# Performance work log

Hardware: AMD Instinct MI355X
Metric: run time of the kernel (lower is better)

The kernel has to match this reference:

```python
import jax, jax.numpy as jnp
import numpy as np

IN_F, T_IN, T_OUT = 8, 96, 32
B = 4096


def _lstm(x, Wih, Whh, b):
    """Standard LSTM (torch gate order i,f,g,o), batch_first. x: [B,T,I] -> [B,T,H].
    Variational dropout with p=0 (eval mode) is identity, so omitted."""
    Bsz = x.shape[0]
    H = Whh.shape[1]
    # precompute input contribution for all timesteps: [B,T,4H]
    xg = jnp.einsum('bti,gi->btg', x, Wih) + b

    def step(carry, xt):
        h, c = carry
        g = xt + h @ Whh.T  # [B,4H]
        i, f, gg, o = jnp.split(g, 4, axis=-1)
        c = jax.nn.sigmoid(f) * c + jax.nn.sigmoid(i) * jnp.tanh(gg)
        h = jax.nn.sigmoid(o) * jnp.tanh(c)
        return (h, c), h

    h0 = jnp.zeros((Bsz, H), x.dtype)
    _, ys = jax.lax.scan(step, (h0, h0), jnp.swapaxes(xg, 0, 1))
    return jnp.swapaxes(ys, 0, 1)


def setup_inputs() -> dict:
    key = jax.random.key(0)
    ks = jax.random.split(key, 16)
    s = 0.1  # init scale
    return {
        'x': jax.random.normal(ks[0], (B, T_IN, IN_F), jnp.float32),
        'e1_Wih': s * jax.random.normal(ks[1], (256, IN_F), jnp.float32),
        'e1_Whh': s * jax.random.normal(ks[2], (256, 64), jnp.float32),
        'e1_b': s * jax.random.normal(ks[3], (256,), jnp.float32),
        'e2_Wih': s * jax.random.normal(ks[4], (4, 64), jnp.float32),
        'e2_Whh': s * jax.random.normal(ks[5], (4, 1), jnp.float32),
        'e2_b': s * jax.random.normal(ks[6], (4,), jnp.float32),
        'd1_Wih': s * jax.random.normal(ks[7], (64, 1), jnp.float32),
        'd1_Whh': s * jax.random.normal(ks[8], (64, 16), jnp.float32),
        'd1_b': s * jax.random.normal(ks[9], (64,), jnp.float32),
        'd2_Wih': s * jax.random.normal(ks[10], (4, 16), jnp.float32),
        'd2_Whh': s * jax.random.normal(ks[11], (4, 1), jnp.float32),
        'd2_b': s * jax.random.normal(ks[12], (4,), jnp.float32),
        'fc1_W': s * jax.random.normal(ks[13], (32, T_IN + T_OUT), jnp.float32),
        'fc1_b': s * jax.random.normal(ks[13], (32,), jnp.float32),
        'fc2_W': s * jax.random.normal(ks[14], (T_OUT, 32), jnp.float32),
        'fc2_b': s * jax.random.normal(ks[15], (T_OUT,), jnp.float32),
    }


def reference(x, e1_Wih, e1_Whh, e1_b, e2_Wih, e2_Whh, e2_b,
              d1_Wih, d1_Whh, d1_b, d2_Wih, d2_Whh, d2_b,
              fc1_W, fc1_b, fc2_W, fc2_b):
    # Encoder: LSTM(in->64) -> LSTM(64->1) -> ReLU
    h = _lstm(x, e1_Wih, e1_Whh, e1_b)
    h = _lstm(h, e2_Wih, e2_Whh, e2_b)
    enc_out = jax.nn.relu(h)  # [B, T_IN, 1]
    # Auxiliary: last T_OUT steps of invocation column (col 0)
    x_aux = x[:, -T_OUT:, 0:1]  # [B, T_OUT, 1]
    dec_in = jnp.concatenate([enc_out, x_aux], axis=1)  # [B, T_IN+T_OUT, 1]
    # Decoder: LSTM(1->16) -> LSTM(16->1)
    d = _lstm(dec_in, d1_Wih, d1_Whh, d1_b)
    d = _lstm(d, d2_Wih, d2_Whh, d2_b)  # [B, T_IN+T_OUT, 1]
    # FC head over the flattened time dim
    flat = d.reshape(-1, T_IN + T_OUT)
    out = flat @ fc1_W.T + fc1_b
    out = out @ fc2_W.T + fc2_b
    return out  # [B, T_OUT]
```

## Files before the change

### kernel.cpp

```cpp
#include <hip/hip_runtime.h>
#include <hip/hip_bf16.h>

typedef __attribute__((ext_vector_type(8))) short bf16x8;
typedef __attribute__((ext_vector_type(4))) float f32x4;

__device__ __forceinline__ float sigm(float x) {
    return __builtin_amdgcn_rcpf(1.0f + __expf(-x));
}
__device__ __forceinline__ float tanh_(float x) {
    float e = __expf(2.0f * x);
    return 1.0f - 2.0f * __builtin_amdgcn_rcpf(e + 1.0f);
}
__device__ __forceinline__ ushort f2bf(float f) {
    uint u = __float_as_uint(f);
    u = u + 0x7FFFu + ((u >> 16) & 1u);
    return (ushort)(u >> 16);
}
__device__ __forceinline__ float bf2f(ushort s) { return __uint_as_float(((uint)s) << 16); }

__global__ __launch_bounds__(1024) __attribute__((amdgpu_waves_per_eu(4, 4)))
void fused_all(
    const float* __restrict__ x,
    const float* __restrict__ e1_Wih, const float* __restrict__ e1_Whh, const float* __restrict__ e1_b,
    const float* __restrict__ e2_Wih, const float* __restrict__ e2_b,
    const float* __restrict__ e2_Whh,
    const float* __restrict__ d1_Wih, const float* __restrict__ d1_Whh, const float* __restrict__ d1_b,
    const float* __restrict__ d2_Wih, const float* __restrict__ d2_b,
    const float* __restrict__ d2_Whh,
    const float* __restrict__ fc1_W, const float* __restrict__ fc1_b,
    const float* __restrict__ fc2_W, const float* __restrict__ fc2_b,
    float* __restrict__ out)
{
    __shared__ float x_s[16 * 772];
    __shared__ __align__(16) ushort h_hi[2][8][16][8];
    __shared__ __align__(16) ushort h_lo[2][8][16][8];
    __shared__ __align__(16) ushort x2_s[2][4][16][8];
    __shared__ __align__(16) float pe2_s[96 * 64];
    __shared__ float din_s[16][132];
    __shared__ float h_lds[16][16];
    __shared__ float pd2_s[16 * 516];
    __shared__ float d2h_s[16 * 132];
    __shared__ float mid_s[16 * 36];

    const int t = threadIdx.x;
    const int bBase = blockIdx.x * 16;
    const int wv = t >> 6, l = t & 63;
    const int row = l & 15, sub = l >> 4;

    for (int bb = 0; bb < 16; ++bb)
        for (int i = t; i < 768; i += 1024)
            x_s[bb * 772 + i] = x[(size_t)(bBase + bb) * 768 + i];

    auto loadW = [&](const float* rowbase, int k0, bool valid, bf16x8& hi8, bf16x8& lo8) {
        float f[8];
        if (valid) {
            float4 v0 = ((const float4*)(rowbase + k0))[0];
            float4 v1 = ((const float4*)(rowbase + k0))[1];
            f[0]=v0.x; f[1]=v0.y; f[2]=v0.z; f[3]=v0.w;
            f[4]=v1.x; f[5]=v1.y; f[6]=v1.z; f[7]=v1.w;
        } else {
            #pragma unroll
            for (int j = 0; j < 8; ++j) f[j] = 0.f;
        }
        #pragma unroll
        for (int j = 0; j < 8; ++j) {
            ushort h = f2bf(f[j]);
            hi8[j] = (short)h;
            lo8[j] = (short)f2bf(f[j] - bf2f(h));
        }
    };
    auto loadA = [&](int T, bool isE2, bf16x8& Ah0, bf16x8& Ah1, bf16x8& Al0, bf16x8& Al1, bf16x8& A2) {
        const int gate = row & 3, uq = row >> 2;
        const bool valid = !isE2 || (uq == 0);
        const int wr = isE2 ? gate : gate * 64 + T * 4 + uq;
        const float* rp = isE2 ? (e2_Wih + (size_t)wr * 64) : (e1_Whh + (size_t)wr * 64);
        loadW(rp, sub * 8,      valid, Ah0, Al0);
        loadW(rp, 32 + sub * 8, valid, Ah1, Al1);
        #pragma unroll
        for (int j = 0; j < 8; ++j) A2[j] = 0;
        if (valid) {
            if (!isE2) {
                if (sub < 3) {
                    const float* wihr = e1_Wih + (size_t)wr * 8;
                    #pragma unroll
                    for (int j = 0; j < 8; ++j) {
                        float f = wihr[j];
                        ushort hh = f2bf(f);
                        A2[j] = (sub < 2) ? (short)hh : (short)f2bf(f - bf2f(hh));
                    }
                } else {
                    float bb = e1_b[wr];
                    ushort hh = f2bf(bb);
                    A2[0] = (short)hh; A2[1] = (short)f2bf(bb - bf2f(hh));
                }
            } else if (sub == 3) {
                float bb = e2_b[wr];
                ushort hh = f2bf(bb);
                A2[0] = (short)hh; A2[1] = (short)f2bf(bb - bf2f(hh));
            }
        }
    };

    bf16x8 A0h0, A0h1, A0l0, A0l1, A0x;
    bf16x8 A2h0, A2h1, A2l0, A2l1, A2x;
    loadA(wv, false, A0h0, A0h1, A0l0, A0l1, A0x);
    if (wv == 15) loadA(0, true, A2h0, A2h1, A2l0, A2l1, A2x);

    __syncthreads();

    if (t < 1024) { ((ushort*)h_hi[0])[t] = 0; ((ushort*)h_lo[0])[t] = 0; }
    if (t < 384) {
        int sb = t >> 7, b = (t >> 3) & 15, j = t & 7;
        float xv = x_s[b * 772 + j];
        ushort hi = f2bf(xv);
        x2_s[0][sb][b][j] = (sb == 1) ? f2bf(xv - bf2f(hi)) : hi;
        x2_s[1][sb][b][j] = 0;
    } else if (t < 512) {
        int b = (t >> 3) & 15, j = t & 7;
        ushort v = (j < 2) ? (ushort)0x3F80 : (ushort)0;
        x2_s[0][3][b][j] = v;
        x2_s[1][3][b][j] = v;
    }

    const int cb = l & 15;
    const int u0_ = wv * 4 + sub;
    float c0r = 0.f;
    __syncthreads();

    #pragma unroll 1
    for (int ts = 0; ts < 96; ++ts) {
        const int p = ts & 1, pn = p ^ 1;

        bf16x8 Bh0 = *(const bf16x8*)&h_hi[p][sub][cb][0];
        bf16x8 Bh1 = *(const bf16x8*)&h_hi[p][4 + sub][cb][0];
        bf16x8 Bl0 = *(const bf16x8*)&h_lo[p][sub][cb][0];
        bf16x8 Bl1 = *(const bf16x8*)&h_lo[p][4 + sub][cb][0];
        bf16x8 Bx  = *(const bf16x8*)&x2_s[p][sub][cb][0];

        f32x4 u0 = {0.f,0.f,0.f,0.f}, v0 = {0.f,0.f,0.f,0.f};
        u0 = __builtin_amdgcn_mfma_f32_16x16x32_bf16(A0h0, Bh0, u0, 0, 0, 0);
        u0 = __builtin_amdgcn_mfma_f32_16x16x32_bf16(A0l0, Bh0, u0, 0, 0, 0);
        u0 = __builtin_amdgcn_mfma_f32_16x16x32_bf16(A0h0, Bl0, u0, 0, 0, 0);
        v0 = __builtin_amdgcn_mfma_f32_16x16x32_bf16(A0h1, Bh1, v0, 0, 0, 0);
        v0 = __builtin_amdgcn_mfma_f32_16x16x32_bf16(A0l1, Bh1, v0, 0, 0, 0);
        v0 = __builtin_amdgcn_mfma_f32_16x16x32_bf16(A0h1, Bl1, v0, 0, 0, 0);
        v0 = __builtin_amdgcn_mfma_f32_16x16x32_bf16(A0x,  Bx,  v0, 0, 0, 0);

        if (wv == 15) {
            f32x4 u2 = {0.f,0.f,0.f,0.f}, v2 = {0.f,0.f,0.f,0.f};
            u2 = __builtin_amdgcn_mfma_f32_16x16x32_bf16(A2h0, Bh0, u2, 0, 0, 0);
            u2 = __builtin_amdgcn_mfma_f32_16x16x32_bf16(A2l0, Bh0, u2, 0, 0, 0);
            u2 = __builtin_amdgcn_mfma_f32_16x16x32_bf16(A2h0, Bl0, u2, 0, 0, 0);
            v2 = __builtin_amdgcn_mfma_f32_16x16x32_bf16(A2h1, Bh1, v2, 0, 0, 0);
            v2 = __builtin_amdgcn_mfma_f32_16x16x32_bf16(A2l1, Bh1, v2, 0, 0, 0);
            v2 = __builtin_amdgcn_mfma_f32_16x16x32_bf16(A2h1, Bl1, v2, 0, 0, 0);
            v2 = __builtin_amdgcn_mfma_f32_16x16x32_bf16(A2x,  Bx,  v2, 0, 0, 0);
            if (ts > 0 && sub == 0) {
                f32x4 acc2 = u2 + v2;
                #pragma unroll
                for (int i = 0; i < 4; ++i)
                    pe2_s[(ts - 1) * 64 + i * 16 + cb] = acc2[i];
            }
        }

        {
            f32x4 acc = u0 + v0;
            c0r = fmaf(sigm(acc[1]), c0r, sigm(acc[0]) * tanh_(acc[2]));
            float hv = sigm(acc[3]) * tanh_(c0r);
            ushort hh = f2bf(hv);
            h_hi[pn][u0_ >> 3][cb][u0_ & 7] = hh;
            h_lo[pn][u0_ >> 3][cb][u0_ & 7] = f2bf(hv - bf2f(hh));
        }

        if (ts < 95 && t < 384) {
            int sb = t >> 7, b = (t >> 3) & 15, j = t & 7;
            float xv = x_s[b * 772 + (ts + 1) * 8 + j];
            ushort hi = f2bf(xv);
            x2_s[pn][sb][b][j] = (sb == 1) ? f2bf(xv - bf2f(hi)) : hi;
        }
        __syncthreads();
    }

    if (wv == 15) {
        bf16x8 Bh0 = *(const bf16x8*)&h_hi[0][sub][cb][0];
        bf16x8 Bh1 = *(const bf16x8*)&h_hi[0][4 + sub][cb][0];
        bf16x8 Bl0 = *(const bf16x8*)&h_lo[0][sub][cb][0];
        bf16x8 Bl1 = *(const bf16x8*)&h_lo[0][4 + sub][cb][0];
        bf16x8 Bx  = *(const bf16x8*)&x2_s[0][sub][cb][0];
        f32x4 u2 = {0.f,0.f,0.f,0.f}, v2 = {0.f,0.f,0.f,0.f};
        u2 = __builtin_amdgcn_mfma_f32_16x16x32_bf16(A2h0, Bh0, u2, 0, 0, 0);
        u2 = __builtin_amdgcn_mfma_f32_16x16x32_bf16(A2l0, Bh0, u2, 0, 0, 0);
        u2 = __builtin_amdgcn_mfma_f32_16x16x32_bf16(A2h0, Bl0, u2, 0, 0, 0);
        v2 = __builtin_amdgcn_mfma_f32_16x16x32_bf16(A2h1, Bh1, v2, 0, 0, 0);
        v2 = __builtin_amdgcn_mfma_f32_16x16x32_bf16(A2l1, Bh1, v2, 0, 0, 0);
        v2 = __builtin_amdgcn_mfma_f32_16x16x32_bf16(A2h1, Bl1, v2, 0, 0, 0);
        v2 = __builtin_amdgcn_mfma_f32_16x16x32_bf16(A2x,  Bx,  v2, 0, 0, 0);
        if (sub == 0) {
            f32x4 acc2 = u2 + v2;
            #pragma unroll
            for (int i = 0; i < 4; ++i)
                pe2_s[95 * 64 + i * 16 + cb] = acc2[i];
        }
    }
    __syncthreads();

    if (wv == 0 && l < 16) {
        const float w0 = e2_Whh[0], w1 = e2_Whh[1], w2 = e2_Whh[2], w3 = e2_Whh[3];
        float ni = pe2_s[l], nf = pe2_s[16 + l], ng = pe2_s[32 + l], no = pe2_s[48 + l];
        float h = 0.f, c = 0.f;
        #pragma unroll 1
        for (int ts = 0; ts < 96; ++ts) {
            float gi = ni, gf = nf, gg2 = ng, go = no;
            if (ts < 95) {
                int b2 = (ts + 1) * 64;
                ni = pe2_s[b2 + l]; nf = pe2_s[b2 + 16 + l];
                ng = pe2_s[b2 + 32 + l]; no = pe2_s[b2 + 48 + l];
            }
            gi = fmaf(h, w0, gi);
            gf = fmaf(h, w1, gf);
            gg2 = fmaf(h, w2, gg2);
            go = fmaf(h, w3, go);
            c = fmaf(sigm(gf), c, sigm(gi) * tanh_(gg2));
            h = sigm(go) * tanh_(c);
            din_s[l][ts] = fmaxf(h, 0.f);
        }
    }
    if (wv >= 1 && wv <= 8) {
        int i = (wv - 1) * 64 + l;
        int B = i >> 5, j = i & 31;
        din_s[B][96 + j] = x_s[B * 772 + (64 + j) * 8];
    }
    __syncthreads();

    {
        const int dw = t >> 6, dlane = t & 63;
        const int dq = dlane >> 4, du = dlane & 15;
        const int drow = dw * 4 + dq;

        if (t < 256) {
            float wih_g[4], bg[4], whh_g[4][16], d2w[16];
            #pragma unroll
            for (int g = 0; g < 4; ++g) {
                wih_g[g] = d1_Wih[g * 16 + du];
                bg[g]    = d1_b[g * 16 + du];
                const float4* wp = (const float4*)(d1_Whh + (size_t)(g * 16 + du) * 16);
                #pragma unroll
                for (int k4 = 0; k4 < 4; ++k4) {
                    float4 v = wp[k4];
                    whh_g[g][4*k4+0] = v.x; whh_g[g][4*k4+1] = v.y;
                    whh_g[g][4*k4+2] = v.z; whh_g[g][4*k4+3] = v.w;
                }
            }
            {
                const float4* wp = (const float4*)(d2_Wih + (size_t)(du & 3) * 16);
                #pragma unroll
                for (int k4 = 0; k4 < 4; ++k4) {
                    float4 v = wp[k4];
                    d2w[4*k4+0] = v.x; d2w[4*k4+1] = v.y; d2w[4*k4+2] = v.z; d2w[4*k4+3] = v.w;
                }
            }
            const float d2bias = d2_b[du & 3];

            float h = 0.f, c = 0.f;
            float hv[16];
            #pragma unroll 1
            for (int ts = 0; ts < 128; ++ts) {
                float xv = din_s[drow][ts];
                float p0 = fmaf(xv, wih_g[0], bg[0]);
                float p1 = fmaf(xv, wih_g[1], bg[1]);
                float p2 = fmaf(xv, wih_g[2], bg[2]);
                float p3 = fmaf(xv, wih_g[3], bg[3]);
                if (ts > 0) {
                    const float4* hp = (const float4*)&h_lds[drow][0];
                    #pragma unroll
                    for (int k4 = 0; k4 < 4; ++k4) {
                        float4 v = hp[k4];
                        hv[4*k4+0] = v.x; hv[4*k4+1] = v.y; hv[4*k4+2] = v.z; hv[4*k4+3] = v.w;
                    }
                    #pragma unroll
                    for (int k = 0; k < 16; ++k) {
                        p0 = fmaf(hv[k], whh_g[0][k], p0);
                        p1 = fmaf(hv[k], whh_g[1][k], p1);
                        p2 = fmaf(hv[k], whh_g[2][k], p2);
                        p3 = fmaf(hv[k], whh_g[3][k], p3);
                    }
                    if (du < 4) {
                        float a = d2bias;
                        #pragma unroll
                        for (int k = 0; k < 16; ++k) a = fmaf(hv[k], d2w[k], a);
                        pd2_s[drow * 516 + (ts - 1) * 4 + du] = a;
                    }
                }
                c = fmaf(sigm(p1), c, sigm(p0) * tanh_(p2));
                h = sigm(p3) * tanh_(c);
                h_lds[drow][du] = h;
            }
            {
                const float4* hp = (const float4*)&h_lds[drow][0];
                #pragma unroll
                for (int k4 = 0; k4 < 4; ++k4) {
                    float4 v = hp[k4];
                    hv[4*k4+0] = v.x; hv[4*k4+1] = v.y; hv[4*k4+2] = v.z; hv[4*k4+3] = v.w;
                }
                if (du < 4) {
                    float a = d2bias;
                    #pragma unroll
                    for (int k = 0; k < 16; ++k) a = fmaf(hv[k], d2w[k], a);
                    pd2_s[drow * 516 + 127 * 4 + du] = a;
                }
            }
        }
        __syncthreads();

        if (t < 16) {
            const float w0 = d2_Whh[0], w1 = d2_Whh[1], w2 = d2_Whh[2], w3 = d2_Whh[3];
            float4 dbuf[4];
            #pragma unroll
            for (int j = 0; j < 4; ++j) dbuf[j] = *(const float4*)&pd2_s[t * 516 + j * 4];
            float h2 = 0.f, c2 = 0.f;
            #pragma unroll
            for (int ts = 0; ts < 128; ++ts) {
                float4 g4 = dbuf[ts & 3];
                if (ts + 4 < 128) dbuf[ts & 3] = *(const float4*)&pd2_s[t * 516 + (ts + 4) * 4];
                float gi = fmaf(h2, w0, g4.x);
                float gf = fmaf(h2, w1, g4.y);
                float gg = fmaf(h2, w2, g4.z);
                float go = fmaf(h2, w3, g4.w);
                c2 = fmaf(sigm(gf), c2, sigm(gi) * tanh_(gg));
                h2 = sigm(go) * tanh_(c2);
                d2h_s[t * 132 + ts] = h2;
            }
        }
        __syncthreads();

        if (t < 256) {
            const int bb = t >> 4, o = t & 15;
            float acc0 = fc1_b[o], acc1 = fc1_b[o + 16];
            const float4* wa = (const float4*)(fc1_W + (size_t)o * 128);
            const float4* wb = (const float4*)(fc1_W + (size_t)(o + 16) * 128);
            const float4* fp = (const float4*)&d2h_s[bb * 132];
            #pragma unroll
            for (int k4 = 0; k4 < 32; ++k4) {
                float4 f = fp[k4], va = wa[k4], vb = wb[k4];
                acc0 = fmaf(f.x, va.x, acc0); acc0 = fmaf(f.y, va.y, acc0);
                acc0 = fmaf(f.z, va.z, acc0); acc0 = fmaf(f.w, va.w, acc0);
                acc1 = fmaf(f.x, vb.x, acc1); acc1 = fmaf(f.y, vb.y, acc1);
                acc1 = fmaf(f.z, vb.z, acc1); acc1 = fmaf(f.w, vb.w, acc1);
            }
            mid_s[bb * 36 + o] = acc0;
            mid_s[bb * 36 + o + 16] = acc1;
        }
        __syncthreads();

        if (t < 256) {
            const int bb = t >> 4, o = t & 15;
            float o0 = fc2_b[o], o1 = fc2_b[o + 16];
            const float4* va2 = (const float4*)(fc2_W + (size_t)o * 32);
            const float4* vb2 = (const float4*)(fc2_W + (size_t)(o + 16) * 32);
            const float4* mp = (const float4*)&mid_s[bb * 36];
            #pragma unroll
            for (int k4 = 0; k4 < 8; ++k4) {
                float4 m = mp[k4], va = va2[k4], vb = vb2[k4];
                o0 = fmaf(m.x, va.x, o0); o0 = fmaf(m.y, va.y, o0);
                o0 = fmaf(m.z, va.z, o0); o0 = fmaf(m.w, va.w, o0);
                o1 = fmaf(m.x, vb.x, o1); o1 = fmaf(m.y, vb.y, o1);
                o1 = fmaf(m.z, vb.z, o1); o1 = fmaf(m.w, vb.w, o1);
            }
            out[((size_t)bBase + bb) * 32 + o] = o0;
            out[((size_t)bBase + bb) * 32 + o + 16] = o1;
        }
    }
}

extern "C" void kernel_launch(void* const* d_in, const int* in_sizes, int n_in,
                              void* d_out, int out_size, void* d_ws, size_t ws_size,
                              hipStream_t stream) {
    const float* x      = (const float*)d_in[0];
    const float* e1_Wih = (const float*)d_in[1];
    const float* e1_Whh = (const float*)d_in[2];
    const float* e1_b   = (const float*)d_in[3];
    const float* e2_Wih = (const float*)d_in[4];
    const float* e2_Whh = (const float*)d_in[5];
    const float* e2_b   = (const float*)d_in[6];
    const float* d1_Wih = (const float*)d_in[7];
    const float* d1_Whh = (const float*)d_in[8];
    const float* d1_b   = (const float*)d_in[9];
    const float* d2_Wih = (const float*)d_in[10];
    const float* d2_Whh = (const float*)d_in[11];
    const float* d2_b   = (const float*)d_in[12];
    const float* fc1_W  = (const float*)d_in[13];
    const float* fc1_b  = (const float*)d_in[14];
    const float* fc2_W  = (const float*)d_in[15];
    const float* fc2_b  = (const float*)d_in[16];
    float* out = (float*)d_out;

    hipLaunchKernelGGL(fused_all, dim3(256), dim3(1024), 0, stream,
                       x, e1_Wih, e1_Whh, e1_b, e2_Wih, e2_b, e2_Whh,
                       d1_Wih, d1_Whh, d1_b, d2_Wih, d2_b, d2_Whh,
                       fc1_W, fc1_b, fc2_W, fc2_b, out);
}
```

Before: 149.7 us.

## Wavefront-pipeline all four LSTM layers in one time loop

```diff
diff --git a/kernel.cpp b/kernel.cpp
--- a/kernel.cpp
+++ b/kernel.cpp
@@ -41,6 +41,7 @@
     __shared__ float pd2_s[16 * 516];
     __shared__ float d2h_s[16 * 132];
     __shared__ float mid_s[16 * 36];
+    __shared__ float w_d1[64][20];
 
     const int t = threadIdx.x;
     const int bBase = blockIdx.x * 16;
@@ -50,6 +51,11 @@
     for (int bb = 0; bb < 16; ++bb)
         for (int i = t; i < 768; i += 1024)
             x_s[bb * 772 + i] = x[(size_t)(bBase + bb) * 768 + i];
+
+    for (int i = t; i < 64 * 18; i += 1024) {
+        int r = i / 18, j = i - r * 18;
+        w_d1[r][j] = (j < 16) ? d1_Whh[r * 16 + j] : ((j == 16) ? d1_Wih[r] : d1_b[r]);
+    }
 
     auto loadW = [&](const float* rowbase, int k0, bool valid, bf16x8& hi8, bf16x8& lo8) {
         float f[8];
@@ -121,254 +127,219 @@
         x2_s[0][3][b][j] = v;
         x2_s[1][3][b][j] = v;
     }
-
-    const int cb = l & 15;
-    const int u0_ = wv * 4 + sub;
-    float c0r = 0.f;
-    __syncthreads();
-
-    #pragma unroll 1
-    for (int ts = 0; ts < 96; ++ts) {
-        const int p = ts & 1, pn = p ^ 1;
-
-        bf16x8 Bh0 = *(const bf16x8*)&h_hi[p][sub][cb][0];
-        bf16x8 Bh1 = *(const bf16x8*)&h_hi[p][4 + sub][cb][0];
-        bf16x8 Bl0 = *(const bf16x8*)&h_lo[p][sub][cb][0];
-        bf16x8 Bl1 = *(const bf16x8*)&h_lo[p][4 + sub][cb][0];
-        bf16x8 Bx  = *(const bf16x8*)&x2_s[p][sub][cb][0];
-
-        f32x4 u0 = {0.f,0.f,0.f,0.f}, v0 = {0.f,0.f,0.f,0.f};
-        u0 = __builtin_amdgcn_mfma_f32_16x16x32_bf16(A0h0, Bh0, u0, 0, 0, 0);
-        u0 = __builtin_amdgcn_mfma_f32_16x16x32_bf16(A0l0, Bh0, u0, 0, 0, 0);
-        u0 = __builtin_amdgcn_mfma_f32_16x16x32_bf16(A0h0, Bl0, u0, 0, 0, 0);
-        v0 = __builtin_amdgcn_mfma_f32_16x16x32_bf16(A0h1, Bh1, v0, 0, 0, 0);
-        v0 = __builtin_amdgcn_mfma_f32_16x16x32_bf16(A0l1, Bh1, v0, 0, 0, 0);
-        v0 = __builtin_amdgcn_mfma_f32_16x16x32_bf16(A0h1, Bl1, v0, 0, 0, 0);
-        v0 = __builtin_amdgcn_mfma_f32_16x16x32_bf16(A0x,  Bx,  v0, 0, 0, 0);
-
-        if (wv == 15) {
-            f32x4 u2 = {0.f,0.f,0.f,0.f}, v2 = {0.f,0.f,0.f,0.f};
-            u2 = __builtin_amdgcn_mfma_f32_16x16x32_bf16(A2h0, Bh0, u2, 0, 0, 0);
-            u2 = __builtin_amdgcn_mfma_f32_16x16x32_bf16(A2l0, Bh0, u2, 0, 0, 0);
-            u2 = __builtin_amdgcn_mfma_f32_16x16x32_bf16(A2h0, Bl0, u2, 0, 0, 0);
-            v2 = __builtin_amdgcn_mfma_f32_16x16x32_bf16(A2h1, Bh1, v2, 0, 0, 0);
-            v2 = __builtin_amdgcn_mfma_f32_16x16x32_bf16(A2l1, Bh1, v2, 0, 0, 0);
-            v2 = __builtin_amdgcn_mfma_f32_16x16x32_bf16(A2h1, Bl1, v2, 0, 0, 0);
-            v2 = __builtin_amdgcn_mfma_f32_16x16x32_bf16(A2x,  Bx,  v2, 0, 0, 0);
-            if (ts > 0 && sub == 0) {
-                f32x4 acc2 = u2 + v2;
-                #pragma unroll
-                for (int i = 0; i < 4; ++i)
-                    pe2_s[(ts - 1) * 64 + i * 16 + cb] = acc2[i];
-            }
-        }
-
-        {
-            f32x4 acc = u0 + v0;
-            c0r = fmaf(sigm(acc[1]), c0r, sigm(acc[0]) * tanh_(acc[2]));
-            float hv = sigm(acc[3]) * tanh_(c0r);
-            ushort hh = f2bf(hv);
-            h_hi[pn][u0_ >> 3][cb][u0_ & 7] = hh;
-            h_lo[pn][u0_ >> 3][cb][u0_ & 7] = f2bf(hv - bf2f(hh));
-        }
-
-        if (ts < 95 && t < 384) {
-            int sb = t >> 7, b = (t >> 3) & 15, j = t & 7;
-            float xv = x_s[b * 772 + (ts + 1) * 8 + j];
-            ushort hi = f2bf(xv);
-            x2_s[pn][sb][b][j] = (sb == 1) ? f2bf(xv - bf2f(hi)) : hi;
-        }
-        __syncthreads();
-    }
-
-    if (wv == 15) {
-        bf16x8 Bh0 = *(const bf16x8*)&h_hi[0][sub][cb][0];
-        bf16x8 Bh1 = *(const bf16x8*)&h_hi[0][4 + sub][cb][0];
-        bf16x8 Bl0 = *(const bf16x8*)&h_lo[0][sub][cb][0];
-        bf16x8 Bl1 = *(const bf16x8*)&h_lo[0][4 + sub][cb][0];
-        bf16x8 Bx  = *(const bf16x8*)&x2_s[0][sub][cb][0];
-        f32x4 u2 = {0.f,0.f,0.f,0.f}, v2 = {0.f,0.f,0.f,0.f};
-        u2 = __builtin_amdgcn_mfma_f32_16x16x32_bf16(A2h0, Bh0, u2, 0, 0, 0);
-        u2 = __builtin_amdgcn_mfma_f32_16x16x32_bf16(A2l0, Bh0, u2, 0, 0, 0);
-        u2 = __builtin_amdgcn_mfma_f32_16x16x32_bf16(A2h0, Bl0, u2, 0, 0, 0);
-        v2 = __builtin_amdgcn_mfma_f32_16x16x32_bf16(A2h1, Bh1, v2, 0, 0, 0);
-        v2 = __builtin_amdgcn_mfma_f32_16x16x32_bf16(A2l1, Bh1, v2, 0, 0, 0);
-        v2 = __builtin_amdgcn_mfma_f32_16x16x32_bf16(A2h1, Bl1, v2, 0, 0, 0);
-        v2 = __builtin_amdgcn_mfma_f32_16x16x32_bf16(A2x,  Bx,  v2, 0, 0, 0);
-        if (sub == 0) {
-            f32x4 acc2 = u2 + v2;
-            #pragma unroll
-            for (int i = 0; i < 4; ++i)
-                pe2_s[95 * 64 + i * 16 + cb] = acc2[i];
-        }
-    }
-    __syncthreads();
-
-    if (wv == 0 && l < 16) {
-        const float w0 = e2_Whh[0], w1 = e2_Whh[1], w2 = e2_Whh[2], w3 = e2_Whh[3];
-        float ni = pe2_s[l], nf = pe2_s[16 + l], ng = pe2_s[32 + l], no = pe2_s[48 + l];
-        float h = 0.f, c = 0.f;
-        #pragma unroll 1
-        for (int ts = 0; ts < 96; ++ts) {
-            float gi = ni, gf = nf, gg2 = ng, go = no;
-            if (ts < 95) {
-                int b2 = (ts + 1) * 64;
-                ni = pe2_s[b2 + l]; nf = pe2_s[b2 + 16 + l];
-                ng = pe2_s[b2 + 32 + l]; no = pe2_s[b2 + 48 + l];
-            }
-            gi = fmaf(h, w0, gi);
-            gf = fmaf(h, w1, gf);
-            gg2 = fmaf(h, w2, gg2);
-            go = fmaf(h, w3, go);
-            c = fmaf(sigm(gf), c, sigm(gi) * tanh_(gg2));
-            h = sigm(go) * tanh_(c);
-            din_s[l][ts] = fmaxf(h, 0.f);
-        }
-    }
     if (wv >= 1 && wv <= 8) {
         int i = (wv - 1) * 64 + l;
         int B = i >> 5, j = i & 31;
         din_s[B][96 + j] = x_s[B * 772 + (64 + j) * 8];
     }
+
+    const int cb = l & 15;
+    const int u0_ = wv * 4 + sub;
+    float c0r = 0.f;
+
+    const float e2w0 = e2_Whh[0], e2w1 = e2_Whh[1], e2w2 = e2_Whh[2], e2w3 = e2_Whh[3];
+    float h_e2 = 0.f, c_e2 = 0.f;
+
+    const float d2r0 = d2_Whh[0], d2r1 = d2_Whh[1], d2r2 = d2_Whh[2], d2r3 = d2_Whh[3];
+    float h_d2 = 0.f, c_d2 = 0.f;
+
+    const int dw = t >> 6, dlane = t & 63;
+    const int dq = dlane >> 4, du = dlane & 15;
+    const int drow = dw * 4 + dq;
+    float d2w[16];
+    float d2bias = 0.f;
+    if (t < 256) {
+        const float4* wp = (const float4*)(d2_Wih + (size_t)(du & 3) * 16);
+        #pragma unroll
+        for (int k4 = 0; k4 < 4; ++k4) {
+            float4 v = wp[k4];
+            d2w[4*k4+0] = v.x; d2w[4*k4+1] = v.y; d2w[4*k4+2] = v.z; d2w[4*k4+3] = v.w;
+        }
+        d2bias = d2_b[du & 3];
+    }
+    float c_d1 = 0.f;
+
     __syncthreads();
 
-    {
-        const int dw = t >> 6, dlane = t & 63;
-        const int dq = dlane >> 4, du = dlane & 15;
-        const int drow = dw * 4 + dq;
-
-        if (t < 256) {
-            float wih_g[4], bg[4], whh_g[4][16], d2w[16];
-            #pragma unroll
-            for (int g = 0; g < 4; ++g) {
-                wih_g[g] = d1_Wih[g * 16 + du];
-                bg[g]    = d1_b[g * 16 + du];
-                const float4* wp = (const float4*)(d1_Whh + (size_t)(g * 16 + du) * 16);
+    #pragma unroll 1
+    for (int it = 0; it < 133; ++it) {
+        const int p = it & 1, pn = p ^ 1;
+
+        if (it <= 96) {
+            bf16x8 Bh0 = *(const bf16x8*)&h_hi[p][sub][cb][0];
+            bf16x8 Bh1 = *(const bf16x8*)&h_hi[p][4 + sub][cb][0];
+            bf16x8 Bl0 = *(const bf16x8*)&h_lo[p][sub][cb][0];
+            bf16x8 Bl1 = *(const bf16x8*)&h_lo[p][4 + sub][cb][0];
+            bf16x8 Bx  = *(const bf16x8*)&x2_s[p][sub][cb][0];
+
+            if (it < 96) {
+                f32x4 u0 = {0.f,0.f,0.f,0.f}, v0 = {0.f,0.f,0.f,0.f};
+                u0 = __builtin_amdgcn_mfma_f32_16x16x32_bf16(A0h0, Bh0, u0, 0, 0, 0);
+                u0 = __builtin_amdgcn_mfma_f32_16x16x32_bf16(A0l0, Bh0, u0, 0, 0, 0);
+                u0 = __builtin_amdgcn_mfma_f32_16x16x32_bf16(A0h0, Bl0, u0, 0, 0, 0);
+                v0 = __builtin_amdgcn_mfma_f32_16x16x32_bf16(A0h1, Bh1, v0, 0, 0, 0);
+                v0 = __builtin_amdgcn_mfma_f32_16x16x32_bf16(A0l1, Bh1, v0, 0, 0, 0);
+                v0 = __builtin_amdgcn_mfma_f32_16x16x32_bf16(A0h1, Bl1, v0, 0, 0, 0);
+                v0 = __builtin_amdgcn_mfma_f32_16x16x32_bf16(A0x,  Bx,  v0, 0, 0, 0);
+
+                f32x4 acc = u0 + v0;
+                c0r = fmaf(sigm(acc[1]), c0r, sigm(acc[0]) * tanh_(acc[2]));
+                float hv = sigm(acc[3]) * tanh_(c0r);
+                ushort hh = f2bf(hv);
+                h_hi[pn][u0_ >> 3][cb][u0_ & 7] = hh;
+                h_lo[pn][u0_ >> 3][cb][u0_ & 7] = f2bf(hv - bf2f(hh));
+            }
+            if (wv == 15) {
+                f32x4 u2 = {0.f,0.f,0.f,0.f}, v2 = {0.f,0.f,0.f,0.f};
+                u2 = __builtin_amdgcn_mfma_f32_16x16x32_bf16(A2h0, Bh0, u2, 0, 0, 0);
+                u2 = __builtin_amdgcn_mfma_f32_16x16x32_bf16(A2l0, Bh0, u2, 0, 0, 0);
+                u2 = __builtin_amdgcn_mfma_f32_16x16x32_bf16(A2h0, Bl0, u2, 0, 0, 0);
+                v2 = __builtin_amdgcn_mfma_f32_16x16x32_bf16(A2h1, Bh1, v2, 0, 0, 0);
+                v2 = __builtin_amdgcn_mfma_f32_16x16x32_bf16(A2l1, Bh1, v2, 0, 0, 0);
+                v2 = __builtin_amdgcn_mfma_f32_16x16x32_bf16(A2h1, Bl1, v2, 0, 0, 0);
+                v2 = __builtin_amdgcn_mfma_f32_16x16x32_bf16(A2x,  Bx,  v2, 0, 0, 0);
+                if (it > 0 && sub == 0) {
+                    f32x4 acc2 = u2 + v2;
+                    #pragma unroll
+                    for (int i = 0; i < 4; ++i)
+                        pe2_s[(it - 1) * 64 + i * 16 + cb] = acc2[i];
+                }
+            }
+            if (it < 95 && t < 384) {
+                int sb = t >> 7, b = (t >> 3) & 15, j = t & 7;
+                float xv = x_s[b * 772 + (it + 1) * 8 + j];
+                ushort hi = f2bf(xv);
+                x2_s[pn][sb][b][j] = (sb == 1) ? f2bf(xv - bf2f(hi)) : hi;
+            }
+        }
+
+        if (wv == 4 && l < 16 && it >= 2 && it <= 97) {
+            int s = it - 2;
+            float gi = pe2_s[s * 64 + l];
+            float gf = pe2_s[s * 64 + 16 + l];
+            float gg = pe2_s[s * 64 + 32 + l];
+            float go = pe2_s[s * 64 + 48 + l];
+            gi = fmaf(h_e2, e2w0, gi);
+            gf = fmaf(h_e2, e2w1, gf);
+            gg = fmaf(h_e2, e2w2, gg);
+            go = fmaf(h_e2, e2w3, go);
+            c_e2 = fmaf(sigm(gf), c_e2, sigm(gi) * tanh_(gg));
+            h_e2 = sigm(go) * tanh_(c_e2);
+            din_s[l][s] = fmaxf(h_e2, 0.f);
+        }
+
+        if (t < 256 && it >= 3 && it <= 130) {
+            int s = it - 3;
+            float xv = din_s[drow][s];
+            float wg0[16], wg1[16], wg2[16], wg3[16];
+            {
+                const float4* w0p = (const float4*)&w_d1[du][0];
+                const float4* w1p = (const float4*)&w_d1[16 + du][0];
+                const float4* w2p = (const float4*)&w_d1[32 + du][0];
+                const float4* w3p = (const float4*)&w_d1[48 + du][0];
                 #pragma unroll
                 for (int k4 = 0; k4 < 4; ++k4) {
-                    float4 v = wp[k4];
-                    whh_g[g][4*k4+0] = v.x; whh_g[g][4*k4+1] = v.y;
-                    whh_g[g][4*k4+2] = v.z; whh_g[g][4*k4+3] = v.w;
-                }
-            }
-            {
-                const float4* wp = (const float4*)(d2_Wih + (size_t)(du & 3) * 16);
-                #pragma unroll
-                for (int k4 = 0; k4 < 4; ++k4) {
-                    float4 v = wp[k4];
-                    d2w[4*k4+0] = v.x; d2w[4*k4+1] = v.y; d2w[4*k4+2] = v.z; d2w[4*k4+3] = v.w;
-                }
-            }
-            const float d2bias = d2_b[du & 3];
-
-            float h = 0.f, c = 0.f;
-            float hv[16];
-            #pragma unroll 1
-            for (int ts = 0; ts < 128; ++ts) {
-                float xv = din_s[drow][ts];
-                float p0 = fmaf(xv, wih_g[0], bg[0]);
-                float p1 = fmaf(xv, wih_g[1], bg[1]);
-                float p2 = fmaf(xv, wih_g[2], bg[2]);
-                float p3 = fmaf(xv, wih_g[3], bg[3]);
-                if (ts > 0) {
-                    const float4* hp = (const float4*)&h_lds[drow][0];
-                    #pragma unroll
-                    for (int k4 = 0; k4 < 4; ++k4) {
-                        float4 v = hp[k4];
-                        hv[4*k4+0] = v.x; hv[4*k4+1] = v.y; hv[4*k4+2] = v.z; hv[4*k4+3] = v.w;
-                    }
-                    #pragma unroll
-                    for (int k = 0; k < 16; ++k) {
-                        p0 = fmaf(hv[k], whh_g[0][k], p0);
-                        p1 = fmaf(hv[k], whh_g[1][k], p1);
-                        p2 = fmaf(hv[k], whh_g[2][k], p2);
-                        p3 = fmaf(hv[k], whh_g[3][k], p3);
-                    }
-                    if (du < 4) {
-                        float a = d2bias;
-                        #pragma unroll
-                        for (int k = 0; k < 16; ++k) a = fmaf(hv[k], d2w[k], a);
-                        pd2_s[drow * 516 + (ts - 1) * 4 + du] = a;
-                    }
-                }
-                c = fmaf(sigm(p1), c, sigm(p0) * tanh_(p2));
-                h = sigm(p3) * tanh_(c);
-                h_lds[drow][du] = h;
-            }
-            {
+                    float4 a = w0p[k4]; wg0[4*k4+0]=a.x; wg0[4*k4+1]=a.y; wg0[4*k4+2]=a.z; wg0[4*k4+3]=a.w;
+                    float4 b = w1p[k4]; wg1[4*k4+0]=b.x; wg1[4*k4+1]=b.y; wg1[4*k4+2]=b.z; wg1[4*k4+3]=b.w;
+                    float4 c4 = w2p[k4]; wg2[4*k4+0]=c4.x; wg2[4*k4+1]=c4.y; wg2[4*k4+2]=c4.z; wg2[4*k4+3]=c4.w;
+                    float4 d4 = w3p[k4]; wg3[4*k4+0]=d4.x; wg3[4*k4+1]=d4.y; wg3[4*k4+2]=d4.z; wg3[4*k4+3]=d4.w;
+                }
+            }
+            float p0 = fmaf(xv, w_d1[du][16],      w_d1[du][17]);
+            float p1 = fmaf(xv, w_d1[16 + du][16], w_d1[16 + du][17]);
+            float p2 = fmaf(xv, w_d1[32 + du][16], w_d1[32 + du][17]);
+            float p3 = fmaf(xv, w_d1[48 + du][16], w_d1[48 + du][17]);
+            if (s > 0) {
+                float hv[16];
                 const float4* hp = (const float4*)&h_lds[drow][0];
                 #pragma unroll
                 for (int k4 = 0; k4 < 4; ++k4) {
                     float4 v = hp[k4];
                     hv[4*k4+0] = v.x; hv[4*k4+1] = v.y; hv[4*k4+2] = v.z; hv[4*k4+3] = v.w;
                 }
+                #pragma unroll
+                for (int k = 0; k < 16; ++k) {
+                    p0 = fmaf(hv[k], wg0[k], p0);
+                    p1 = fmaf(hv[k], wg1[k], p1);
+                    p2 = fmaf(hv[k], wg2[k], p2);
+                    p3 = fmaf(hv[k], wg3[k], p3);
+                }
                 if (du < 4) {
                     float a = d2bias;
                     #pragma unroll
                     for (int k = 0; k < 16; ++k) a = fmaf(hv[k], d2w[k], a);
-                    pd2_s[drow * 516 + 127 * 4 + du] = a;
-                }
-            }
-        }
+                    pd2_s[drow * 516 + (s - 1) * 4 + du] = a;
+                }
+            }
+            c_d1 = fmaf(sigm(p1), c_d1, sigm(p0) * tanh_(p2));
+            float h = sigm(p3) * tanh_(c_d1);
+            h_lds[drow][du] = h;
+        }
+        if (t < 256 && it == 131) {
+            float hv[16];
+            const float4* hp = (const float4*)&h_lds[drow][0];
+            #pragma unroll
+            for (int k4 = 0; k4 < 4; ++k4) {
+                float4 v = hp[k4];
+                hv[4*k4+0] = v.x; hv[4*k4+1] = v.y; hv[4*k4+2] = v.z; hv[4*k4+3] = v.w;
+            }
+            if (du < 4) {
+                float a = d2bias;
+                #pragma unroll
+                for (int k = 0; k < 16; ++k) a = fmaf(hv[k], d2w[k], a);
+                pd2_s[drow * 516 + 127 * 4 + du] = a;
+            }
+        }
+
+        if (wv == 5 && l < 16 && it >= 5) {
+            int s = it - 5;
+            float4 g4 = *(const float4*)&pd2_s[l * 516 + s * 4];
+            float gi = fmaf(h_d2, d2r0, g4.x);
+            float gf = fmaf(h_d2, d2r1, g4.y);
+            float gg = fmaf(h_d2, d2r2, g4.z);
+            float go = fmaf(h_d2, d2r3, g4.w);
+            c_d2 = fmaf(sigm(gf), c_d2, sigm(gi) * tanh_(gg));
+            h_d2 = sigm(go) * tanh_(c_d2);
+            d2h_s[l * 132 + s] = h_d2;
+        }
+
         __syncthreads();
-
-        if (t < 16) {
-            const float w0 = d2_Whh[0], w1 = d2_Whh[1], w2 = d2_Whh[2], w3 = d2_Whh[3];
-            float4 dbuf[4];
-            #pragma unroll
-            for (int j = 0; j < 4; ++j) dbuf[j] = *(const float4*)&pd2_s[t * 516 + j * 4];
-            float h2 = 0.f, c2 = 0.f;
-            #pragma unroll
-            for (int ts = 0; ts < 128; ++ts) {
-                float4 g4 = dbuf[ts & 3];
-                if (ts + 4 < 128) dbuf[ts & 3] = *(const float4*)&pd2_s[t * 516 + (ts + 4) * 4];
-                float gi = fmaf(h2, w0, g4.x);
-                float gf = fmaf(h2, w1, g4.y);
-                float gg = fmaf(h2, w2, g4.z);
-                float go = fmaf(h2, w3, g4.w);
-                c2 = fmaf(sigm(gf), c2, sigm(gi) * tanh_(gg));
-                h2 = sigm(go) * tanh_(c2);
-                d2h_s[t * 132 + ts] = h2;
-            }
-        }
-        __syncthreads();
-
-        if (t < 256) {
-            const int bb = t >> 4, o = t & 15;
-            float acc0 = fc1_b[o], acc1 = fc1_b[o + 16];
-            const float4* wa = (const float4*)(fc1_W + (size_t)o * 128);
-            const float4* wb = (const float4*)(fc1_W + (size_t)(o + 16) * 128);
-            const float4* fp = (const float4*)&d2h_s[bb * 132];
-            #pragma unroll
-            for (int k4 = 0; k4 < 32; ++k4) {
-                float4 f = fp[k4], va = wa[k4], vb = wb[k4];
-                acc0 = fmaf(f.x, va.x, acc0); acc0 = fmaf(f.y, va.y, acc0);
-                acc0 = fmaf(f.z, va.z, acc0); acc0 = fmaf(f.w, va.w, acc0);
-                acc1 = fmaf(f.x, vb.x, acc1); acc1 = fmaf(f.y, vb.y, acc1);
-                acc1 = fmaf(f.z, vb.z, acc1); acc1 = fmaf(f.w, vb.w, acc1);
-            }
-            mid_s[bb * 36 + o] = acc0;
-            mid_s[bb * 36 + o + 16] = acc1;
-        }
-        __syncthreads();
-
-        if (t < 256) {
-            const int bb = t >> 4, o = t & 15;
-            float o0 = fc2_b[o], o1 = fc2_b[o + 16];
-            const float4* va2 = (const float4*)(fc2_W + (size_t)o * 32);
-            const float4* vb2 = (const float4*)(fc2_W + (size_t)(o + 16) * 32);
-            const float4* mp = (const float4*)&mid_s[bb * 36];
-            #pragma unroll
-            for (int k4 = 0; k4 < 8; ++k4) {
-                float4 m = mp[k4], va = va2[k4], vb = vb2[k4];
-                o0 = fmaf(m.x, va.x, o0); o0 = fmaf(m.y, va.y, o0);
-                o0 = fmaf(m.z, va.z, o0); o0 = fmaf(m.w, va.w, o0);
-                o1 = fmaf(m.x, vb.x, o1); o1 = fmaf(m.y, vb.y, o1);
-                o1 = fmaf(m.z, vb.z, o1); o1 = fmaf(m.w, vb.w, o1);
-            }
-            out[((size_t)bBase + bb) * 32 + o] = o0;
-            out[((size_t)bBase + bb) * 32 + o + 16] = o1;
-        }
+    }
+
+    if (t < 256) {
+        const int bb = t >> 4, o = t & 15;
+        float acc0 = fc1_b[o], acc1 = fc1_b[o + 16];
+        const float4* wa = (const float4*)(fc1_W + (size_t)o * 128);
+        const float4* wb = (const float4*)(fc1_W + (size_t)(o + 16) * 128);
+        const float4* fp = (const float4*)&d2h_s[bb * 132];
+        #pragma unroll
+        for (int k4 = 0; k4 < 32; ++k4) {
+            float4 f = fp[k4], va = wa[k4], vb = wb[k4];
+            acc0 = fmaf(f.x, va.x, acc0); acc0 = fmaf(f.y, va.y, acc0);
+            acc0 = fmaf(f.z, va.z, acc0); acc0 = fmaf(f.w, va.w, acc0);
+            acc1 = fmaf(f.x, vb.x, acc1); acc1 = fmaf(f.y, vb.y, acc1);
+            acc1 = fmaf(f.z, vb.z, acc1); acc1 = fmaf(f.w, vb.w, acc1);
+        }
+        mid_s[bb * 36 + o] = acc0;
+        mid_s[bb * 36 + o + 16] = acc1;
+    }
+    __syncthreads();
+    if (t < 256) {
+        const int bb = t >> 4, o = t & 15;
+        float o0 = fc2_b[o], o1 = fc2_b[o + 16];
+        const float4* va2 = (const float4*)(fc2_W + (size_t)o * 32);
+        const float4* vb2 = (const float4*)(fc2_W + (size_t)(o + 16) * 32);
+        const float4* mp = (const float4*)&mid_s[bb * 36];
+        #pragma unroll
+        for (int k4 = 0; k4 < 8; ++k4) {
+            float4 m = mp[k4], va = va2[k4], vb = vb2[k4];
+            o0 = fmaf(m.x, va.x, o0); o0 = fmaf(m.y, va.y, o0);
+            o0 = fmaf(m.z, va.z, o0); o0 = fmaf(m.w, va.w, o0);
+            o1 = fmaf(m.x, vb.x, o1); o1 = fmaf(m.y, vb.y, o1);
+            o1 = fmaf(m.z, vb.z, o1); o1 = fmaf(m.w, vb.w, o1);
+        }
+        out[((size_t)bBase + bb) * 32 + o] = o0;
+        out[((size_t)bBase + bb) * 32 + o + 16] = o1;
     }
 }
 
```

After: 369.8 us. 2.47x slower.
